# Optimization experiments

Measured on AMD Instinct MI355X. Metric: run time of the kernel, lower is better.

Reference implementation:

```python
import jax, jax.numpy as jnp
import numpy as np

B, N, F_DIM = 64, 4096, 64
K_SLOTS, D, N_ITERS = 8, 64, 3
EPS = 1e-8
LN_EPS = 1e-5  # torch LayerNorm default


def layernorm(x, g, b):
    mu = jnp.mean(x, axis=-1, keepdims=True)
    var = jnp.mean(jnp.square(x - mu), axis=-1, keepdims=True)
    return (x - mu) * jax.lax.rsqrt(var + LN_EPS) * g + b


def gru_cell(x, h, w_ih, w_hh, b_ih, b_hh):
    # torch.nn.GRUCell semantics; weights are [3D, D] with gate order r, z, n
    gi = x @ w_ih.T + b_ih
    gh = h @ w_hh.T + b_hh
    i_r, i_z, i_n = jnp.split(gi, 3, axis=-1)
    h_r, h_z, h_n = jnp.split(gh, 3, axis=-1)
    r = jax.nn.sigmoid(i_r + h_r)
    z = jax.nn.sigmoid(i_z + h_z)
    n = jnp.tanh(i_n + r * h_n)
    return (1.0 - z) * n + z * h


def setup_inputs() -> dict:
    key = jax.random.key(0)
    ks = jax.random.split(key, 16)
    f32 = jnp.float32
    s = 0.05  # small init scale for weights
    return {
        "inputs": jax.random.normal(ks[0], (B, N, F_DIM), f32),
        "slots_noise": jax.random.normal(ks[1], (B, K_SLOTS, D), f32),
        "slots_mu": jax.random.normal(ks[2], (1, 1, D), f32) * s,
        "slots_log_sigma": jax.random.normal(ks[3], (1, 1, D), f32) * s,
        "Wq": jax.random.normal(ks[4], (D, D), f32) * s,
        "Wk": jax.random.normal(ks[5], (D, F_DIM), f32) * s,
        "Wv": jax.random.normal(ks[6], (D, F_DIM), f32) * s,
        "gru_w_ih": jax.random.normal(ks[7], (3 * D, D), f32) * s,
        "gru_w_hh": jax.random.normal(ks[8], (3 * D, D), f32) * s,
        "gru_b_ih": jnp.zeros((3 * D,), f32),
        "gru_b_hh": jnp.zeros((3 * D,), f32),
        "mlp_w1": jax.random.normal(ks[9], (2 * D, D), f32) * s,
        "mlp_b1": jnp.zeros((2 * D,), f32),
        "mlp_w2": jax.random.normal(ks[10], (D, 2 * D), f32) * s,
        "mlp_b2": jnp.zeros((D,), f32),
        "ln_in_g": jnp.ones((F_DIM,), f32), "ln_in_b": jnp.zeros((F_DIM,), f32),
        "ln_slots_g": jnp.ones((D,), f32), "ln_slots_b": jnp.zeros((D,), f32),
        "ln_mlp_g": jnp.ones((D,), f32), "ln_mlp_b": jnp.zeros((D,), f32),
    }


def reference(inputs, slots_noise, slots_mu, slots_log_sigma, Wq, Wk, Wv,
              gru_w_ih, gru_w_hh, gru_b_ih, gru_b_hh,
              mlp_w1, mlp_b1, mlp_w2, mlp_b2,
              ln_in_g, ln_in_b, ln_slots_g, ln_slots_b, ln_mlp_g, ln_mlp_b):
    x = layernorm(inputs, ln_in_g, ln_in_b)          # [B, N, F]
    k = jnp.einsum('bnf,df->bnd', x, Wk)             # [B, N, D]
    v = jnp.einsum('bnf,df->bnd', x, Wv)             # [B, N, D]

    slots = slots_mu + jnp.exp(slots_log_sigma) * slots_noise  # [B, K, D]
    scale = D ** -0.5

    for _ in range(N_ITERS):
        slots_prev = slots
        s_n = layernorm(slots, ln_slots_g, ln_slots_b)
        q = jnp.einsum('bkd,ed->bke', s_n, Wq)                  # [B, K, D]
        attn_logits = jnp.einsum('bnd,bkd->bnk', k, q) * scale  # [B, N, K]
        attn = jax.nn.softmax(attn_logits, axis=-1) + EPS       # softmax over slots
        attn = attn / jnp.sum(attn, axis=1, keepdims=True)      # renormalize over N
        updates = jnp.einsum('bnk,bnd->bkd', attn, v)           # [B, K, D]
        slots = gru_cell(updates.reshape(-1, D), slots_prev.reshape(-1, D),
                         gru_w_ih, gru_w_hh, gru_b_ih, gru_b_hh).reshape(B, K_SLOTS, D)
        h = layernorm(slots, ln_mlp_g, ln_mlp_b)
        h = jax.nn.relu(h @ mlp_w1.T + mlp_b1) @ mlp_w2.T + mlp_b2
        slots = slots + h
    return slots
```

## Files before the change

### kernel.cpp

```cpp
#include <hip/hip_runtime.h>
#include <math.h>

#define NN 4096
#define LN_EPS 1e-5f
#define EPS 1e-8f

typedef unsigned short ushortT;
typedef unsigned int uintT;
typedef __attribute__((ext_vector_type(8))) short short8;
typedef __attribute__((ext_vector_type(4))) float f32x4;
typedef __attribute__((ext_vector_type(4))) unsigned short us4;

#define OFF_KT    0L
#define OFF_V     16777216L
#define OFF_QT    33554432L
#define OFF_PART  33587200L
#define OFF_PCOL  34111488L
#define OFF_SLOTS 34119680L
#define OFF_WIHT  34152448L
#define OFF_WHHT  34164736L
#define OFF_W1T   34177024L
#define OFF_W2T   34185216L
#define OFF_WQT   34193408L
#define OFF_WKV   34197504L
#define OFF_CNT   34201600L

__device__ __forceinline__ float wredsum(float v) {
#pragma unroll
  for (int off = 32; off > 0; off >>= 1) v += __shfl_xor(v, off);
  return v;
}

__device__ __forceinline__ ushortT f2bf(float f) {
  uintT b = __float_as_uint(f);
  b += 0x7fff + ((b >> 16) & 1);
  return (ushortT)(b >> 16);
}

__global__ __launch_bounds__(256) void k_setup(
    const float* __restrict__ w_ih, const float* __restrict__ w_hh,
    const float* __restrict__ w1, const float* __restrict__ w2,
    const float* __restrict__ Wq,
    const float* __restrict__ Wk, const float* __restrict__ Wv,
    const float* __restrict__ noise, const float* __restrict__ smu,
    const float* __restrict__ slsig,
    const float* __restrict__ g_sl, const float* __restrict__ b_sl,
    float* __restrict__ wihT, float* __restrict__ whhT,
    float* __restrict__ w1T, float* __restrict__ w2T, float* __restrict__ wqT,
    ushortT* __restrict__ wpack,
    float* __restrict__ slots, ushortT* __restrict__ qF,
    int* __restrict__ cnt)
{
  const int tid = threadIdx.x;
  int idx = blockIdx.x * 256 + tid;
  if (idx < 12288) {
    int j = idx >> 6, f = idx & 63;
    wihT[f * 192 + j] = w_ih[idx];
  } else if (idx < 24576) {
    int i = idx - 12288; int j = i >> 6, f = i & 63;
    whhT[f * 192 + j] = w_hh[i];
  } else if (idx < 32768) {
    int i = idx - 24576; int j = i >> 6, f = i & 63;
    w1T[f * 128 + j] = w1[i];
  } else if (idx < 40960) {
    int i = idx - 32768; int d = i >> 7, j = i & 127;
    w2T[j * 64 + d] = w2[i];
  } else if (idx < 45056) {
    int i = idx - 40960; int e = i >> 6, d = i & 63;
    wqT[d * 64 + e] = Wq[i];
  } else if (idx < 53248) {
    int i = idx - 45056;
    int j = i & 7, l = (i >> 3) & 63, t2 = i >> 9;
    int ct = t2 >> 1, kb = t2 & 1;
    int kf = kb * 32 + ((l >> 4) << 3) + j;
    int col = (ct << 4) | (l & 15);
    float val = (col < 64) ? Wk[col * 64 + kf] : Wv[(col - 64) * 64 + kf];
    wpack[i] = f2bf(val);
  }

  if (blockIdx.x >= 128) {
    if (blockIdx.x < 136) cnt[(blockIdx.x - 128) * 256 + tid] = 0;
    return;
  }

  __shared__ float WqS[64 * 65];
  __shared__ float S[4][64];
  const int lane = tid & 63, wave = tid >> 6;
  const int row = blockIdx.x * 4 + wave;
  const int b = row >> 3, ks = row & 7;

#pragma unroll
  for (int i = 0; i < 16; ++i) {
    int ii = tid + i * 256;
    int e = ii >> 6, d = ii & 63;
    WqS[d * 65 + e] = Wq[ii];
  }

  float s0 = fmaf(expf(slsig[lane]), noise[row * 64 + lane], smu[lane]);
  slots[row * 64 + lane] = s0;

  float mu = wredsum(s0) * (1.f / 64.f);
  float dx = s0 - mu;
  float var = wredsum(dx * dx) * (1.f / 64.f);
  float sn = dx * rsqrtf(var + LN_EPS) * g_sl[lane] + b_sl[lane];
  S[wave][lane] = sn;
  __syncthreads();
  float qe = 0.f;
#pragma unroll 16
  for (int d = 0; d < 64; ++d) qe = fmaf(S[wave][d], WqS[d * 65 + lane], qe);
  const int kb = lane >> 5, lrow = (lane & 31) >> 3, j = lane & 7;
  qF[((((b * 2 + kb) << 6) + (lrow << 4) + ks) << 3) + j] = f2bf(qe * 0.125f);
  qF[((((b * 2 + kb) << 6) + (lrow << 4) + 8 + ks) << 3) + j] = 0;
}

__global__ __launch_bounds__(256, 4) void k_ln_project(
    const float* __restrict__ inp, const ushortT* __restrict__ wpack,
    const float* __restrict__ g, const float* __restrict__ bbv,
    ushortT* __restrict__ ktF, ushortT* __restrict__ vF)
{
  __shared__ __align__(16) ushortT xnF[4096];
  __shared__ __align__(16) ushortT kS[4096];
  const int tid = threadIdx.x;
  const int lane = tid & 63;
  const int wave = tid >> 6;
  const int l15 = lane & 15, q = lane >> 4;
  const int tile = blockIdx.x;
  const int b = tile >> 6;
  const int c = tile & 63;
  const int n0 = c << 6;
  const float* rowbase = inp + (((long)b * NN + n0) << 6);
  const float4 g4 = *(const float4*)&g[l15 << 2];
  const float4 b4 = *(const float4*)&bbv[l15 << 2];

#pragma unroll
  for (int i = 0; i < 4; ++i) {
    const int row = (wave << 4) + (i << 2) + q;
    float4 x = *(const float4*)&rowbase[(row << 6) + (l15 << 2)];
    float s = x.x + x.y + x.z + x.w;
    float s2 = fmaf(x.x, x.x, fmaf(x.y, x.y, fmaf(x.z, x.z, x.w * x.w)));
    s += __shfl_xor(s, 1);  s2 += __shfl_xor(s2, 1);
    s += __shfl_xor(s, 2);  s2 += __shfl_xor(s2, 2);
    s += __shfl_xor(s, 4);  s2 += __shfl_xor(s2, 4);
    s += __shfl_xor(s, 8);  s2 += __shfl_xor(s2, 8);
    const float mu = s * (1.f / 64.f);
    const float var = fmaf(-mu, mu, s2 * (1.f / 64.f));
    const float rs = rsqrtf(var + LN_EPS);
    us4 p = {f2bf((x.x - mu) * rs * g4.x + b4.x), f2bf((x.y - mu) * rs * g4.y + b4.y),
             f2bf((x.z - mu) * rs * g4.z + b4.z), f2bf((x.w - mu) * rs * g4.w + b4.w)};
    *(us4*)&xnF[((((wave << 1) + (l15 >> 3)) << 6) + (((l15 & 7) >> 1) << 4)
                 + (row & 15)) * 8 + ((l15 & 1) << 2)] = p;
  }

  short8 bfrag[2][2];
#pragma unroll
  for (int nt = 0; nt < 2; ++nt)
#pragma unroll
    for (int kb = 0; kb < 2; ++kb)
      bfrag[nt][kb] = *(const short8*)&wpack[((((2 * wave + nt) << 1) | kb) * 64 + lane) << 3];

  __syncthreads();

  f32x4 acc[4][2];
#pragma unroll
  for (int mt = 0; mt < 4; ++mt)
#pragma unroll
    for (int nt = 0; nt < 2; ++nt) acc[mt][nt] = (f32x4){0.f, 0.f, 0.f, 0.f};

#pragma unroll
  for (int mt = 0; mt < 4; ++mt) {
    short8 a0 = *(const short8*)&xnF[((mt * 2 + 0) * 64 + lane) << 3];
    short8 a1 = *(const short8*)&xnF[((mt * 2 + 1) * 64 + lane) << 3];
#pragma unroll
    for (int nt = 0; nt < 2; ++nt) {
      acc[mt][nt] = __builtin_amdgcn_mfma_f32_16x16x32_bf16(a0, bfrag[nt][0], acc[mt][nt], 0, 0, 0);
      acc[mt][nt] = __builtin_amdgcn_mfma_f32_16x16x32_bf16(a1, bfrag[nt][1], acc[mt][nt], 0, 0, 0);
    }
  }

  if (wave < 2) {
#pragma unroll
    for (int mt = 0; mt < 4; ++mt)
#pragma unroll
      for (int nt = 0; nt < 2; ++nt) {
        const int base = (((mt * 2 + wave) << 6) + ((2 * nt + (l15 >> 3)) << 4) + (q << 2));
#pragma unroll
        for (int r = 0; r < 4; ++r)
          kS[((base + r) << 3) + (l15 & 7)] = f2bf(acc[mt][nt][r]);
      }
  } else {
    ushortT* vbase = vF + ((long)(b * 64 + c) << 12);
#pragma unroll
    for (int mt = 0; mt < 4; ++mt)
#pragma unroll
      for (int nt = 0; nt < 2; ++nt) {
        const int ntg = 2 * (wave - 2) + nt;
        us4 p = {f2bf(acc[mt][nt][0]), f2bf(acc[mt][nt][1]),
                 f2bf(acc[mt][nt][2]), f2bf(acc[mt][nt][3])};
        *(us4*)&vbase[(((((ntg << 1) + (mt >> 1)) << 6)
                        + (((mt & 1) * 2 + (q >> 1)) << 4) + l15) << 3)
                      + ((q & 1) << 2)] = p;
      }
  }
  __syncthreads();

  ushortT* kdst = ktF + ((long)(b * 64 + c) << 12);
  short8 v0 = *(const short8*)&kS[tid << 4];
  short8 v1 = *(const short8*)&kS[(tid << 4) + 8];
  *(short8*)&kdst[tid << 4] = v0;
  *(short8*)&kdst[(tid << 4) + 8] = v1;
}

__global__ __launch_bounds__(256, 4) void k_attn_fused(
    const ushortT* __restrict__ ktF, const ushortT* __restrict__ vF,
    ushortT* __restrict__ qF,
    float* __restrict__ part, float* __restrict__ pcol, int* __restrict__ cnt,
    float* __restrict__ slots,
    const float* __restrict__ wihT, const float* __restrict__ whhT,
    const float* __restrict__ w1T, const float* __restrict__ w2T,
    const float* __restrict__ wqT,
    const float* __restrict__ b_ih, const float* __restrict__ b_hh,
    const float* __restrict__ mb1, const float* __restrict__ mb2,
    const float* __restrict__ g_ml, const float* __restrict__ b_ml,
    const float* __restrict__ g_sl, const float* __restrict__ b_sl,
    float* __restrict__ dout, int it)
{
  __shared__ __align__(16) ushortT attnF[4][1024];
  __shared__ float redLds[4][512];
  __shared__ float colLds[4][8];
  __shared__ int flagS;
  const int tid = threadIdx.x;
  const int lane = tid & 63;
  const int wave = tid >> 6;
  const int l15 = lane & 15, q = lane >> 4;
  const int b = blockIdx.x >> 4;
  const int i16 = blockIdx.x & 15;
  const int chunk = (i16 << 2) | wave;

  const ushortT* kbF = ktF + ((long)(b * 64 + chunk) << 12);
  const ushortT* vbF = vF + ((long)(b * 64 + chunk) << 12);

  short8 qB[2];
#pragma unroll
  for (int kb = 0; kb < 2; ++kb)
    qB[kb] = *(const short8*)&qF[(((b * 2 + kb) << 6) + lane) << 3];
  short8 kA[4][2];
#pragma unroll
  for (int mt = 0; mt < 4; ++mt)
#pragma unroll
    for (int kb = 0; kb < 2; ++kb)
      kA[mt][kb] = *(const short8*)&kbF[((mt * 2 + kb) * 64 + lane) << 3];
  short8 vB[4][2];
#pragma unroll
  for (int nt = 0; nt < 4; ++nt)
#pragma unroll
    for (int ks = 0; ks < 2; ++ks)
      vB[nt][ks] = *(const short8*)&vbF[((nt * 2 + ks) * 64 + lane) << 3];

  f32x4 accL[4];
#pragma unroll
  for (int mt = 0; mt < 4; ++mt) {
    accL[mt] = (f32x4){0.f, 0.f, 0.f, 0.f};
    accL[mt] = __builtin_amdgcn_mfma_f32_16x16x32_bf16(kA[mt][0], qB[0], accL[mt], 0, 0, 0);
    accL[mt] = __builtin_amdgcn_mfma_f32_16x16x32_bf16(kA[mt][1], qB[1], accL[mt], 0, 0, 0);
  }

  float csum = 0.f;
#pragma unroll
  for (int mt = 0; mt < 4; ++mt) {
    float av[4];
#pragma unroll
    for (int r = 0; r < 4; ++r) {
      float ev = __expf(accL[mt][r]);
      float sv = ev;
      sv += __shfl_xor(sv, 1); sv += __shfl_xor(sv, 2); sv += __shfl_xor(sv, 4);
      float a = ev * (1.f / sv) + EPS;
      av[r] = a;
      csum += a;
    }
    us4 p = {f2bf(av[0]), f2bf(av[1]), f2bf(av[2]), f2bf(av[3])};
    *(us4*)&attnF[wave][((((mt >> 1) << 6) + (((mt & 1) * 2 + (q >> 1)) << 4)
                          + l15) << 3) + ((q & 1) << 2)] = p;
  }
  csum += __shfl_xor(csum, 16);
  csum += __shfl_xor(csum, 32);

  short8 pA0 = *(const short8*)&attnF[wave][(0 * 64 + lane) << 3];
  short8 pA1 = *(const short8*)&attnF[wave][(1 * 64 + lane) << 3];

  f32x4 accP[4];
#pragma unroll
  for (int nt = 0; nt < 4; ++nt) {
    accP[nt] = (f32x4){0.f, 0.f, 0.f, 0.f};
    accP[nt] = __builtin_amdgcn_mfma_f32_16x16x32_bf16(pA0, vB[nt][0], accP[nt], 0, 0, 0);
    accP[nt] = __builtin_amdgcn_mfma_f32_16x16x32_bf16(pA1, vB[nt][1], accP[nt], 0, 0, 0);
  }

  float (*accLds)[8][64] = (float (*)[8][64])redLds;
  if (q < 2) {
#pragma unroll
    for (int nt = 0; nt < 4; ++nt)
#pragma unroll
      for (int r = 0; r < 4; ++r)
        accLds[wave][q * 4 + r][nt * 16 + l15] = accP[nt][r];
  }
  if (q == 0 && l15 < 8) colLds[wave][l15] = csum;
  __syncthreads();

  float* myPart = part + ((long)(b * 16 + i16) << 9);
#pragma unroll
  for (int r = 0; r < 2; ++r) {
    const int o = tid + r * 256;
    const int kk = o >> 6, d = o & 63;
    float s = accLds[0][kk][d] + accLds[1][kk][d] + accLds[2][kk][d] + accLds[3][kk][d];
    __hip_atomic_store(&myPart[o], s, __ATOMIC_RELAXED, __HIP_MEMORY_SCOPE_AGENT);
  }
  if (tid < 8) {
    float s = colLds[0][tid] + colLds[1][tid] + colLds[2][tid] + colLds[3][tid];
    __hip_atomic_store(&pcol[(b * 16 + i16) * 8 + tid], s,
                       __ATOMIC_RELAXED, __HIP_MEMORY_SCOPE_AGENT);
  }

  asm volatile("s_waitcnt vmcnt(0) lgkmcnt(0)" ::: "memory");
  __syncthreads();
  if (tid == 0) {
    int old = atomicAdd(&cnt[b << 5], 1);
    flagS = (old == it * 16 + 15);
  }
  __syncthreads();
  if (!flagS) return;

  float* accR = (float*)&attnF[0][0];
  float* csR  = accR + 512;
  const float* partB = part + ((long)b << 13);
#pragma unroll
  for (int r = 0; r < 2; ++r) {
    const int o = tid + r * 256;
    float s = 0.f;
#pragma unroll
    for (int i = 0; i < 16; ++i)
      s += __hip_atomic_load(&partB[(i << 9) + o], __ATOMIC_RELAXED, __HIP_MEMORY_SCOPE_AGENT);
    accR[o] = s;
  }
  if (tid < 8) {
    float s = 0.f;
#pragma unroll
    for (int i = 0; i < 16; ++i)
      s += __hip_atomic_load(&pcol[(b * 16 + i) * 8 + tid], __ATOMIC_RELAXED, __HIP_MEMORY_SCOPE_AGENT);
    csR[tid] = s;
  }
  __syncthreads();

  float* SwA = &redLds[wave][0];
  float* SwB = &redLds[wave][256];
  const int ksA = wave * 2, ksB = ksA + 1;
  const int rowA = b * 8 + ksA, rowB = b * 8 + ksB;

  const float bir = b_ih[lane], biz = b_ih[64 + lane], bin_ = b_ih[128 + lane];
  const float bhr = b_hh[lane], bhz = b_hh[64 + lane], bhn = b_hh[128 + lane];
  const float m1a = mb1[lane], m1b = mb1[64 + lane];
  const float m2v = mb2[lane];
  const float gml = g_ml[lane], bml = b_ml[lane];
  const float gsl = g_sl[lane], bsl = b_sl[lane];

  const float u0 = accR[ksA * 64 + lane] / csR[ksA];
  const float u1 = accR[ksB * 64 + lane] / csR[ksB];
  const float h0 = slots[rowA * 64 + lane];
  const float h1 = slots[rowB * 64 + lane];
  SwA[lane] = u0; SwA[64 + lane] = h0;
  SwB[lane] = u1; SwB[64 + lane] = h1;

  float gir0 = bir, giz0 = biz, gin0 = bin_, ghr0 = bhr, ghz0 = bhz, ghn0 = bhn;
  float gir1 = bir, giz1 = biz, gin1 = bin_, ghr1 = bhr, ghz1 = bhz, ghn1 = bhn;
#pragma unroll 8
  for (int f = 0; f < 64; ++f) {
    const float wr = wihT[f * 192 + lane], wz = wihT[f * 192 + 64 + lane],
                wn = wihT[f * 192 + 128 + lane];
    const float vr = whhT[f * 192 + lane], vz = whhT[f * 192 + 64 + lane],
                vn = whhT[f * 192 + 128 + lane];
    const float uA = SwA[f], hA = SwA[64 + f];
    const float uB = SwB[f], hB = SwB[64 + f];
    gir0 = fmaf(uA, wr, gir0); giz0 = fmaf(uA, wz, giz0); gin0 = fmaf(uA, wn, gin0);
    ghr0 = fmaf(hA, vr, ghr0); ghz0 = fmaf(hA, vz, ghz0); ghn0 = fmaf(hA, vn, ghn0);
    gir1 = fmaf(uB, wr, gir1); giz1 = fmaf(uB, wz, giz1); gin1 = fmaf(uB, wn, gin1);
    ghr1 = fmaf(hB, vr, ghr1); ghz1 = fmaf(hB, vz, ghz1); ghn1 = fmaf(hB, vn, ghn1);
  }
  const float r0 = 1.f / (1.f + expf(-(gir0 + ghr0)));
  const float z0 = 1.f / (1.f + expf(-(giz0 + ghz0)));
  const float n0v = tanhf(fmaf(r0, ghn0, gin0));
  const float hnew0 = (1.f - z0) * n0v + z0 * h0;
  const float r1 = 1.f / (1.f + expf(-(gir1 + ghr1)));
  const float z1 = 1.f / (1.f + expf(-(giz1 + ghz1)));
  const float n1v = tanhf(fmaf(r1, ghn1, gin1));
  const float hnew1 = (1.f - z1) * n1v + z1 * h1;

  float sa = hnew0, sb = hnew1;
#pragma unroll
  for (int off = 32; off > 0; off >>= 1) { sa += __shfl_xor(sa, off); sb += __shfl_xor(sb, off); }
  const float muA = sa * (1.f / 64.f), muB = sb * (1.f / 64.f);
  float dxA = hnew0 - muA, dxB = hnew1 - muB;
  float va = dxA * dxA, vb = dxB * dxB;
#pragma unroll
  for (int off = 32; off > 0; off >>= 1) { va += __shfl_xor(va, off); vb += __shfl_xor(vb, off); }
  SwA[128 + lane] = dxA * rsqrtf(va * (1.f / 64.f) + LN_EPS) * gml + bml;
  SwB[128 + lane] = dxB * rsqrtf(vb * (1.f / 64.f) + LN_EPS) * gml + bml;

  float h1a0 = m1a, h1b0 = m1b, h1a1 = m1a, h1b1 = m1b;
#pragma unroll 8
  for (int f = 0; f < 64; ++f) {
    const float wA = w1T[f * 128 + lane], wB = w1T[f * 128 + 64 + lane];
    const float lA = SwA[128 + f], lB = SwB[128 + f];
    h1a0 = fmaf(lA, wA, h1a0); h1b0 = fmaf(lA, wB, h1b0);
    h1a1 = fmaf(lB, wA, h1a1); h1b1 = fmaf(lB, wB, h1b1);
  }
  SwA[lane] = fmaxf(h1a0, 0.f); SwA[64 + lane] = fmaxf(h1b0, 0.f);
  SwB[lane] = fmaxf(h1a1, 0.f); SwB[64 + lane] = fmaxf(h1b1, 0.f);

  float o0 = m2v, o1 = m2v;
#pragma unroll 8
  for (int j = 0; j < 128; ++j) {
    const float w = w2T[j * 64 + lane];
    o0 = fmaf(SwA[j], w, o0);
    o1 = fmaf(SwB[j], w, o1);
  }
  const float snew0 = hnew0 + o0;
  const float snew1 = hnew1 + o1;
  slots[rowA * 64 + lane] = snew0;
  slots[rowB * 64 + lane] = snew1;
  if (dout) { dout[rowA * 64 + lane] = snew0; dout[rowB * 64 + lane] = snew1; }

  float ta = snew0, tb = snew1;
#pragma unroll
  for (int off = 32; off > 0; off >>= 1) { ta += __shfl_xor(ta, off); tb += __shfl_xor(tb, off); }
  const float mu2A = ta * (1.f / 64.f), mu2B = tb * (1.f / 64.f);
  float d2A = snew0 - mu2A, d2B = snew1 - mu2B;
  float v2a = d2A * d2A, v2b = d2B * d2B;
#pragma unroll
  for (int off = 32; off > 0; off >>= 1) { v2a += __shfl_xor(v2a, off); v2b += __shfl_xor(v2b, off); }
  SwA[128 + lane] = d2A * rsqrtf(v2a * (1.f / 64.f) + LN_EPS) * gsl + bsl;
  SwB[128 + lane] = d2B * rsqrtf(v2b * (1.f / 64.f) + LN_EPS) * gsl + bsl;

  float qe0 = 0.f, qe1 = 0.f;
#pragma unroll 8
  for (int d = 0; d < 64; ++d) {
    const float w = wqT[d * 64 + lane];
    qe0 = fmaf(SwA[128 + d], w, qe0);
    qe1 = fmaf(SwB[128 + d], w, qe1);
  }
  const int kb = lane >> 5, lrow = (lane & 31) >> 3, j = lane & 7;
  qF[((((b * 2 + kb) << 6) + (lrow << 4) + ksA) << 3) + j] = f2bf(qe0 * 0.125f);
  qF[((((b * 2 + kb) << 6) + (lrow << 4) + ksB) << 3) + j] = f2bf(qe1 * 0.125f);
}

extern "C" void kernel_launch(void* const* d_in, const int* in_sizes, int n_in,
                              void* d_out, int out_size, void* d_ws, size_t ws_size,
                              hipStream_t stream) {
  const float* inp   = (const float*)d_in[0];
  const float* noise = (const float*)d_in[1];
  const float* smu   = (const float*)d_in[2];
  const float* slsig = (const float*)d_in[3];
  const float* Wq    = (const float*)d_in[4];
  const float* Wk    = (const float*)d_in[5];
  const float* Wv    = (const float*)d_in[6];
  const float* w_ih  = (const float*)d_in[7];
  const float* w_hh  = (const float*)d_in[8];
  const float* b_ih  = (const float*)d_in[9];
  const float* b_hh  = (const float*)d_in[10];
  const float* w1    = (const float*)d_in[11];
  const float* b1    = (const float*)d_in[12];
  const float* w2    = (const float*)d_in[13];
  const float* b2    = (const float*)d_in[14];
  const float* g_in  = (const float*)d_in[15];
  const float* bi_in = (const float*)d_in[16];
  const float* g_sl  = (const float*)d_in[17];
  const float* bi_sl = (const float*)d_in[18];
  const float* g_ml  = (const float*)d_in[19];
  const float* bi_ml = (const float*)d_in[20];

  float* ws      = (float*)d_ws;
  ushortT* ktF   = (ushortT*)(ws + OFF_KT);
  ushortT* vF    = (ushortT*)(ws + OFF_V);
  ushortT* qF    = (ushortT*)(ws + OFF_QT);
  float* part    = ws + OFF_PART;
  float* pcol    = ws + OFF_PCOL;
  float* sl      = ws + OFF_SLOTS;
  float* wihT    = ws + OFF_WIHT;
  float* whhT    = ws + OFF_WHHT;
  float* w1T     = ws + OFF_W1T;
  float* w2T     = ws + OFF_W2T;
  float* wqT     = ws + OFF_WQT;
  ushortT* wpk   = (ushortT*)(ws + OFF_WKV);
  int* cnt       = (int*)(ws + OFF_CNT);

  k_setup<<<208, 256, 0, stream>>>(w_ih, w_hh, w1, w2, Wq, Wk, Wv,
                                   noise, smu, slsig, g_sl, bi_sl,
                                   wihT, whhT, w1T, w2T, wqT, wpk,
                                   sl, qF, cnt);
  k_ln_project<<<4096, 256, 0, stream>>>(inp, wpk, g_in, bi_in, ktF, vF);
  for (int it = 0; it < 3; ++it) {
    k_attn_fused<<<1024, 256, 0, stream>>>(ktF, vF, qF, part, pcol, cnt, sl,
                                           wihT, whhT, w1T, w2T, wqT,
                                           b_ih, b_hh, b1, b2, g_ml, bi_ml, g_sl, bi_sl,
                                           it == 2 ? (float*)d_out : nullptr, it);
  }
}
```

Baseline: 250.5 us.

## Fuse three slot-attention iterations into one persistent kernel with per-batch flags

Result: slower. 438.9 us (+75.2%).

```diff
diff --git a/kernel.cpp b/kernel.cpp
--- a/kernel.cpp
+++ b/kernel.cpp
@@ -79,7 +79,7 @@
   }
 
   if (blockIdx.x >= 128) {
-    if (blockIdx.x < 136) cnt[(blockIdx.x - 128) * 256 + tid] = 0;
+    if (blockIdx.x < 144) cnt[(blockIdx.x - 128) * 256 + tid] = 0;
     return;
   }
 
@@ -210,9 +210,9 @@
   *(short8*)&kdst[(tid << 4) + 8] = v1;
 }
 
-__global__ __launch_bounds__(256, 4) void k_attn_fused(
+__global__ __launch_bounds__(256, 4) void k_attn_iter(
     const ushortT* __restrict__ ktF, const ushortT* __restrict__ vF,
-    ushortT* __restrict__ qF,
+    const ushortT* __restrict__ qF,
     float* __restrict__ part, float* __restrict__ pcol, int* __restrict__ cnt,
     float* __restrict__ slots,
     const float* __restrict__ wihT, const float* __restrict__ whhT,
@@ -222,7 +222,7 @@
     const float* __restrict__ mb1, const float* __restrict__ mb2,
     const float* __restrict__ g_ml, const float* __restrict__ b_ml,
     const float* __restrict__ g_sl, const float* __restrict__ b_sl,
-    float* __restrict__ dout, int it)
+    float* __restrict__ dout)
 {
   __shared__ __align__(16) ushortT attnF[4][1024];
   __shared__ float redLds[4][512];
@@ -238,11 +238,10 @@
 
   const ushortT* kbF = ktF + ((long)(b * 64 + chunk) << 12);
   const ushortT* vbF = vF + ((long)(b * 64 + chunk) << 12);
-
-  short8 qB[2];
-#pragma unroll
-  for (int kb = 0; kb < 2; ++kb)
-    qB[kb] = *(const short8*)&qF[(((b * 2 + kb) << 6) + lane) << 3];
+  int* cnt_b = &cnt[b << 5];
+  int* flg_b = &cnt[2048 + (b << 5)];
+  const float gsl = g_sl[lane], bsl = b_sl[lane];
+
   short8 kA[4][2];
 #pragma unroll
   for (int mt = 0; mt < 4; ++mt)
@@ -256,199 +255,245 @@
     for (int ks = 0; ks < 2; ++ks)
       vB[nt][ks] = *(const short8*)&vbF[((nt * 2 + ks) * 64 + lane) << 3];
 
-  f32x4 accL[4];
-#pragma unroll
-  for (int mt = 0; mt < 4; ++mt) {
-    accL[mt] = (f32x4){0.f, 0.f, 0.f, 0.f};
-    accL[mt] = __builtin_amdgcn_mfma_f32_16x16x32_bf16(kA[mt][0], qB[0], accL[mt], 0, 0, 0);
-    accL[mt] = __builtin_amdgcn_mfma_f32_16x16x32_bf16(kA[mt][1], qB[1], accL[mt], 0, 0, 0);
-  }
-
-  float csum = 0.f;
-#pragma unroll
-  for (int mt = 0; mt < 4; ++mt) {
-    float av[4];
-#pragma unroll
-    for (int r = 0; r < 4; ++r) {
-      float ev = __expf(accL[mt][r]);
-      float sv = ev;
-      sv += __shfl_xor(sv, 1); sv += __shfl_xor(sv, 2); sv += __shfl_xor(sv, 4);
-      float a = ev * (1.f / sv) + EPS;
-      av[r] = a;
-      csum += a;
-    }
-    us4 p = {f2bf(av[0]), f2bf(av[1]), f2bf(av[2]), f2bf(av[3])};
-    *(us4*)&attnF[wave][((((mt >> 1) << 6) + (((mt & 1) * 2 + (q >> 1)) << 4)
-                          + l15) << 3) + ((q & 1) << 2)] = p;
-  }
-  csum += __shfl_xor(csum, 16);
-  csum += __shfl_xor(csum, 32);
-
-  short8 pA0 = *(const short8*)&attnF[wave][(0 * 64 + lane) << 3];
-  short8 pA1 = *(const short8*)&attnF[wave][(1 * 64 + lane) << 3];
-
-  f32x4 accP[4];
-#pragma unroll
-  for (int nt = 0; nt < 4; ++nt) {
-    accP[nt] = (f32x4){0.f, 0.f, 0.f, 0.f};
-    accP[nt] = __builtin_amdgcn_mfma_f32_16x16x32_bf16(pA0, vB[nt][0], accP[nt], 0, 0, 0);
-    accP[nt] = __builtin_amdgcn_mfma_f32_16x16x32_bf16(pA1, vB[nt][1], accP[nt], 0, 0, 0);
-  }
-
-  float (*accLds)[8][64] = (float (*)[8][64])redLds;
-  if (q < 2) {
-#pragma unroll
-    for (int nt = 0; nt < 4; ++nt)
-#pragma unroll
-      for (int r = 0; r < 4; ++r)
-        accLds[wave][q * 4 + r][nt * 16 + l15] = accP[nt][r];
-  }
-  if (q == 0 && l15 < 8) colLds[wave][l15] = csum;
-  __syncthreads();
-
-  float* myPart = part + ((long)(b * 16 + i16) << 9);
-#pragma unroll
-  for (int r = 0; r < 2; ++r) {
-    const int o = tid + r * 256;
-    const int kk = o >> 6, d = o & 63;
-    float s = accLds[0][kk][d] + accLds[1][kk][d] + accLds[2][kk][d] + accLds[3][kk][d];
-    __hip_atomic_store(&myPart[o], s, __ATOMIC_RELAXED, __HIP_MEMORY_SCOPE_AGENT);
-  }
-  if (tid < 8) {
-    float s = colLds[0][tid] + colLds[1][tid] + colLds[2][tid] + colLds[3][tid];
-    __hip_atomic_store(&pcol[(b * 16 + i16) * 8 + tid], s,
-                       __ATOMIC_RELAXED, __HIP_MEMORY_SCOPE_AGENT);
-  }
-
-  asm volatile("s_waitcnt vmcnt(0) lgkmcnt(0)" ::: "memory");
-  __syncthreads();
-  if (tid == 0) {
-    int old = atomicAdd(&cnt[b << 5], 1);
-    flagS = (old == it * 16 + 15);
-  }
-  __syncthreads();
-  if (!flagS) return;
-
-  float* accR = (float*)&attnF[0][0];
-  float* csR  = accR + 512;
-  const float* partB = part + ((long)b << 13);
-#pragma unroll
-  for (int r = 0; r < 2; ++r) {
-    const int o = tid + r * 256;
-    float s = 0.f;
-#pragma unroll
-    for (int i = 0; i < 16; ++i)
-      s += __hip_atomic_load(&partB[(i << 9) + o], __ATOMIC_RELAXED, __HIP_MEMORY_SCOPE_AGENT);
-    accR[o] = s;
-  }
-  if (tid < 8) {
-    float s = 0.f;
-#pragma unroll
-    for (int i = 0; i < 16; ++i)
-      s += __hip_atomic_load(&pcol[(b * 16 + i) * 8 + tid], __ATOMIC_RELAXED, __HIP_MEMORY_SCOPE_AGENT);
-    csR[tid] = s;
-  }
-  __syncthreads();
-
-  float* SwA = &redLds[wave][0];
-  float* SwB = &redLds[wave][256];
-  const int ksA = wave * 2, ksB = ksA + 1;
-  const int rowA = b * 8 + ksA, rowB = b * 8 + ksB;
-
-  const float bir = b_ih[lane], biz = b_ih[64 + lane], bin_ = b_ih[128 + lane];
-  const float bhr = b_hh[lane], bhz = b_hh[64 + lane], bhn = b_hh[128 + lane];
-  const float m1a = mb1[lane], m1b = mb1[64 + lane];
-  const float m2v = mb2[lane];
-  const float gml = g_ml[lane], bml = b_ml[lane];
-  const float gsl = g_sl[lane], bsl = b_sl[lane];
-
-  const float u0 = accR[ksA * 64 + lane] / csR[ksA];
-  const float u1 = accR[ksB * 64 + lane] / csR[ksB];
-  const float h0 = slots[rowA * 64 + lane];
-  const float h1 = slots[rowB * 64 + lane];
-  SwA[lane] = u0; SwA[64 + lane] = h0;
-  SwB[lane] = u1; SwB[64 + lane] = h1;
-
-  float gir0 = bir, giz0 = biz, gin0 = bin_, ghr0 = bhr, ghz0 = bhz, ghn0 = bhn;
-  float gir1 = bir, giz1 = biz, gin1 = bin_, ghr1 = bhr, ghz1 = bhz, ghn1 = bhn;
+  for (int it = 0; it < 3; ++it) {
+    short8 qB[2];
+    if (it == 0) {
+#pragma unroll
+      for (int kb = 0; kb < 2; ++kb)
+        qB[kb] = *(const short8*)&qF[(((b * 2 + kb) << 6) + lane) << 3];
+    } else {
+      if (tid == 0) {
+        while (__hip_atomic_load(flg_b, __ATOMIC_RELAXED, __HIP_MEMORY_SCOPE_AGENT) < it)
+          __builtin_amdgcn_s_sleep(2);
+      }
+      __syncthreads();
+      float* qsq  = &redLds[0][0];
+      float* qLds = &redLds[2][0];
+      const int ksA = wave * 2, ksB = ksA + 1;
+      float sA = __hip_atomic_load(&slots[(b * 8 + ksA) * 64 + lane],
+                                   __ATOMIC_RELAXED, __HIP_MEMORY_SCOPE_AGENT);
+      float sB = __hip_atomic_load(&slots[(b * 8 + ksB) * 64 + lane],
+                                   __ATOMIC_RELAXED, __HIP_MEMORY_SCOPE_AGENT);
+      float ta = sA, tb = sB;
+#pragma unroll
+      for (int off = 32; off > 0; off >>= 1) { ta += __shfl_xor(ta, off); tb += __shfl_xor(tb, off); }
+      const float muA = ta * (1.f / 64.f), muB = tb * (1.f / 64.f);
+      const float dxA = sA - muA, dxB = sB - muB;
+      float va = dxA * dxA, vb = dxB * dxB;
+#pragma unroll
+      for (int off = 32; off > 0; off >>= 1) { va += __shfl_xor(va, off); vb += __shfl_xor(vb, off); }
+      qsq[ksA * 64 + lane] = dxA * rsqrtf(va * (1.f / 64.f) + LN_EPS) * gsl + bsl;
+      qsq[ksB * 64 + lane] = dxB * rsqrtf(vb * (1.f / 64.f) + LN_EPS) * gsl + bsl;
+      __syncthreads();
+      float qeA = 0.f, qeB = 0.f;
 #pragma unroll 8
-  for (int f = 0; f < 64; ++f) {
-    const float wr = wihT[f * 192 + lane], wz = wihT[f * 192 + 64 + lane],
-                wn = wihT[f * 192 + 128 + lane];
-    const float vr = whhT[f * 192 + lane], vz = whhT[f * 192 + 64 + lane],
-                vn = whhT[f * 192 + 128 + lane];
-    const float uA = SwA[f], hA = SwA[64 + f];
-    const float uB = SwB[f], hB = SwB[64 + f];
-    gir0 = fmaf(uA, wr, gir0); giz0 = fmaf(uA, wz, giz0); gin0 = fmaf(uA, wn, gin0);
-    ghr0 = fmaf(hA, vr, ghr0); ghz0 = fmaf(hA, vz, ghz0); ghn0 = fmaf(hA, vn, ghn0);
-    gir1 = fmaf(uB, wr, gir1); giz1 = fmaf(uB, wz, giz1); gin1 = fmaf(uB, wn, gin1);
-    ghr1 = fmaf(hB, vr, ghr1); ghz1 = fmaf(hB, vz, ghz1); ghn1 = fmaf(hB, vn, ghn1);
-  }
-  const float r0 = 1.f / (1.f + expf(-(gir0 + ghr0)));
-  const float z0 = 1.f / (1.f + expf(-(giz0 + ghz0)));
-  const float n0v = tanhf(fmaf(r0, ghn0, gin0));
-  const float hnew0 = (1.f - z0) * n0v + z0 * h0;
-  const float r1 = 1.f / (1.f + expf(-(gir1 + ghr1)));
-  const float z1 = 1.f / (1.f + expf(-(giz1 + ghz1)));
-  const float n1v = tanhf(fmaf(r1, ghn1, gin1));
-  const float hnew1 = (1.f - z1) * n1v + z1 * h1;
-
-  float sa = hnew0, sb = hnew1;
-#pragma unroll
-  for (int off = 32; off > 0; off >>= 1) { sa += __shfl_xor(sa, off); sb += __shfl_xor(sb, off); }
-  const float muA = sa * (1.f / 64.f), muB = sb * (1.f / 64.f);
-  float dxA = hnew0 - muA, dxB = hnew1 - muB;
-  float va = dxA * dxA, vb = dxB * dxB;
-#pragma unroll
-  for (int off = 32; off > 0; off >>= 1) { va += __shfl_xor(va, off); vb += __shfl_xor(vb, off); }
-  SwA[128 + lane] = dxA * rsqrtf(va * (1.f / 64.f) + LN_EPS) * gml + bml;
-  SwB[128 + lane] = dxB * rsqrtf(vb * (1.f / 64.f) + LN_EPS) * gml + bml;
-
-  float h1a0 = m1a, h1b0 = m1b, h1a1 = m1a, h1b1 = m1b;
+      for (int d = 0; d < 64; ++d) {
+        const float w = wqT[d * 64 + lane];
+        qeA = fmaf(qsq[ksA * 64 + d], w, qeA);
+        qeB = fmaf(qsq[ksB * 64 + d], w, qeB);
+      }
+      qLds[ksA * 64 + lane] = qeA * 0.125f;
+      qLds[ksB * 64 + lane] = qeB * 0.125f;
+      __syncthreads();
+#pragma unroll
+      for (int kb = 0; kb < 2; ++kb) {
+        short8 v = (short8){0, 0, 0, 0, 0, 0, 0, 0};
+        if (l15 < 8) {
+          const int e0 = (kb << 5) + (q << 3);
+          float4 f0 = *(const float4*)&qLds[l15 * 64 + e0];
+          float4 f1 = *(const float4*)&qLds[l15 * 64 + e0 + 4];
+          v[0] = (short)f2bf(f0.x); v[1] = (short)f2bf(f0.y);
+          v[2] = (short)f2bf(f0.z); v[3] = (short)f2bf(f0.w);
+          v[4] = (short)f2bf(f1.x); v[5] = (short)f2bf(f1.y);
+          v[6] = (short)f2bf(f1.z); v[7] = (short)f2bf(f1.w);
+        }
+        qB[kb] = v;
+      }
+      __syncthreads();
+    }
+
+    f32x4 accL[4];
+#pragma unroll
+    for (int mt = 0; mt < 4; ++mt) {
+      accL[mt] = (f32x4){0.f, 0.f, 0.f, 0.f};
+      accL[mt] = __builtin_amdgcn_mfma_f32_16x16x32_bf16(kA[mt][0], qB[0], accL[mt], 0, 0, 0);
+      accL[mt] = __builtin_amdgcn_mfma_f32_16x16x32_bf16(kA[mt][1], qB[1], accL[mt], 0, 0, 0);
+    }
+
+    float csum = 0.f;
+#pragma unroll
+    for (int mt = 0; mt < 4; ++mt) {
+      float av[4];
+#pragma unroll
+      for (int r = 0; r < 4; ++r) {
+        float ev = __expf(accL[mt][r]);
+        float sv = ev;
+        sv += __shfl_xor(sv, 1); sv += __shfl_xor(sv, 2); sv += __shfl_xor(sv, 4);
+        float a = ev * (1.f / sv) + EPS;
+        av[r] = a;
+        csum += a;
+      }
+      us4 p = {f2bf(av[0]), f2bf(av[1]), f2bf(av[2]), f2bf(av[3])};
+      *(us4*)&attnF[wave][((((mt >> 1) << 6) + (((mt & 1) * 2 + (q >> 1)) << 4)
+                            + l15) << 3) + ((q & 1) << 2)] = p;
+    }
+    csum += __shfl_xor(csum, 16);
+    csum += __shfl_xor(csum, 32);
+
+    short8 pA0 = *(const short8*)&attnF[wave][(0 * 64 + lane) << 3];
+    short8 pA1 = *(const short8*)&attnF[wave][(1 * 64 + lane) << 3];
+
+    f32x4 accP[4];
+#pragma unroll
+    for (int nt = 0; nt < 4; ++nt) {
+      accP[nt] = (f32x4){0.f, 0.f, 0.f, 0.f};
+      accP[nt] = __builtin_amdgcn_mfma_f32_16x16x32_bf16(pA0, vB[nt][0], accP[nt], 0, 0, 0);
+      accP[nt] = __builtin_amdgcn_mfma_f32_16x16x32_bf16(pA1, vB[nt][1], accP[nt], 0, 0, 0);
+    }
+
+    float (*accLds)[8][64] = (float (*)[8][64])redLds;
+    if (q < 2) {
+#pragma unroll
+      for (int nt = 0; nt < 4; ++nt)
+#pragma unroll
+        for (int r = 0; r < 4; ++r)
+          accLds[wave][q * 4 + r][nt * 16 + l15] = accP[nt][r];
+    }
+    if (q == 0 && l15 < 8) colLds[wave][l15] = csum;
+    __syncthreads();
+
+    float* myPart = part + ((long)(b * 16 + i16) << 9);
+#pragma unroll
+    for (int r = 0; r < 2; ++r) {
+      const int o = tid + r * 256;
+      const int kk = o >> 6, d = o & 63;
+      float s = accLds[0][kk][d] + accLds[1][kk][d] + accLds[2][kk][d] + accLds[3][kk][d];
+      __hip_atomic_store(&myPart[o], s, __ATOMIC_RELAXED, __HIP_MEMORY_SCOPE_AGENT);
+    }
+    if (tid < 8) {
+      float s = colLds[0][tid] + colLds[1][tid] + colLds[2][tid] + colLds[3][tid];
+      __hip_atomic_store(&pcol[(b * 16 + i16) * 8 + tid], s,
+                         __ATOMIC_RELAXED, __HIP_MEMORY_SCOPE_AGENT);
+    }
+
+    asm volatile("s_waitcnt vmcnt(0) lgkmcnt(0)" ::: "memory");
+    __syncthreads();
+    if (tid == 0) {
+      int old = atomicAdd(cnt_b, 1);
+      flagS = (old == it * 16 + 15);
+    }
+    __syncthreads();
+
+    if (flagS) {
+      float* accR = (float*)&attnF[0][0];
+      float* csR  = accR + 512;
+      const float* partB = part + ((long)b << 13);
+#pragma unroll
+      for (int r = 0; r < 2; ++r) {
+        const int o = tid + r * 256;
+        float s = 0.f;
+#pragma unroll
+        for (int i = 0; i < 16; ++i)
+          s += __hip_atomic_load(&partB[(i << 9) + o], __ATOMIC_RELAXED, __HIP_MEMORY_SCOPE_AGENT);
+        accR[o] = s;
+      }
+      if (tid < 8) {
+        float s = 0.f;
+#pragma unroll
+        for (int i = 0; i < 16; ++i)
+          s += __hip_atomic_load(&pcol[(b * 16 + i) * 8 + tid], __ATOMIC_RELAXED, __HIP_MEMORY_SCOPE_AGENT);
+        csR[tid] = s;
+      }
+      __syncthreads();
+
+      float* SwA = &redLds[wave][0];
+      float* SwB = &redLds[wave][256];
+      const int ksA = wave * 2, ksB = ksA + 1;
+      const int rowA = b * 8 + ksA, rowB = b * 8 + ksB;
+
+      const float bir = b_ih[lane], biz = b_ih[64 + lane], bin_ = b_ih[128 + lane];
+      const float bhr = b_hh[lane], bhz = b_hh[64 + lane], bhn = b_hh[128 + lane];
+      const float m1a = mb1[lane], m1b = mb1[64 + lane];
+      const float m2v = mb2[lane];
+      const float gml = g_ml[lane], bml = b_ml[lane];
+
+      const float u0 = accR[ksA * 64 + lane] / csR[ksA];
+      const float u1 = accR[ksB * 64 + lane] / csR[ksB];
+      const float h0 = __hip_atomic_load(&slots[rowA * 64 + lane], __ATOMIC_RELAXED, __HIP_MEMORY_SCOPE_AGENT);
+      const float h1 = __hip_atomic_load(&slots[rowB * 64 + lane], __ATOMIC_RELAXED, __HIP_MEMORY_SCOPE_AGENT);
+      SwA[lane] = u0; SwA[64 + lane] = h0;
+      SwB[lane] = u1; SwB[64 + lane] = h1;
+
+      float gir0 = bir, giz0 = biz, gin0 = bin_, ghr0 = bhr, ghz0 = bhz, ghn0 = bhn;
+      float gir1 = bir, giz1 = biz, gin1 = bin_, ghr1 = bhr, ghz1 = bhz, ghn1 = bhn;
 #pragma unroll 8
-  for (int f = 0; f < 64; ++f) {
-    const float wA = w1T[f * 128 + lane], wB = w1T[f * 128 + 64 + lane];
-    const float lA = SwA[128 + f], lB = SwB[128 + f];
-    h1a0 = fmaf(lA, wA, h1a0); h1b0 = fmaf(lA, wB, h1b0);
-    h1a1 = fmaf(lB, wA, h1a1); h1b1 = fmaf(lB, wB, h1b1);
-  }
-  SwA[lane] = fmaxf(h1a0, 0.f); SwA[64 + lane] = fmaxf(h1b0, 0.f);
-  SwB[lane] = fmaxf(h1a1, 0.f); SwB[64 + lane] = fmaxf(h1b1, 0.f);
-
-  float o0 = m2v, o1 = m2v;
+      for (int f = 0; f < 64; ++f) {
+        const float wr = wihT[f * 192 + lane], wz = wihT[f * 192 + 64 + lane],
+                    wn = wihT[f * 192 + 128 + lane];
+        const float vr = whhT[f * 192 + lane], vz = whhT[f * 192 + 64 + lane],
+                    vn = whhT[f * 192 + 128 + lane];
+        const float uA = SwA[f], hA = SwA[64 + f];
+        const float uB = SwB[f], hB = SwB[64 + f];
+        gir0 = fmaf(uA, wr, gir0); giz0 = fmaf(uA, wz, giz0); gin0 = fmaf(uA, wn, gin0);
+        ghr0 = fmaf(hA, vr, ghr0); ghz0 = fmaf(hA, vz, ghz0); ghn0 = fmaf(hA, vn, ghn0);
+        gir1 = fmaf(uB, wr, gir1); giz1 = fmaf(uB, wz, giz1); gin1 = fmaf(uB, wn, gin1);
+        ghr1 = fmaf(hB, vr, ghr1); ghz1 = fmaf(hB, vz, ghz1); ghn1 = fmaf(hB, vn, ghn1);
+      }
+      const float r0 = 1.f / (1.f + expf(-(gir0 + ghr0)));
+      const float z0 = 1.f / (1.f + expf(-(giz0 + ghz0)));
+      const float n0v = tanhf(fmaf(r0, ghn0, gin0));
+      const float hnew0 = (1.f - z0) * n0v + z0 * h0;
+      const float r1 = 1.f / (1.f + expf(-(gir1 + ghr1)));
+      const float z1 = 1.f / (1.f + expf(-(giz1 + ghz1)));
+      const float n1v = tanhf(fmaf(r1, ghn1, gin1));
+      const float hnew1 = (1.f - z1) * n1v + z1 * h1;
+
+      float sa = hnew0, sb = hnew1;
+#pragma unroll
+      for (int off = 32; off > 0; off >>= 1) { sa += __shfl_xor(sa, off); sb += __shfl_xor(sb, off); }
+      const float muA = sa * (1.f / 64.f), muB = sb * (1.f / 64.f);
+      float dxA = hnew0 - muA, dxB = hnew1 - muB;
+      float va = dxA * dxA, vb = dxB * dxB;
+#pragma unroll
+      for (int off = 32; off > 0; off >>= 1) { va += __shfl_xor(va, off); vb += __shfl_xor(vb, off); }
+      SwA[128 + lane] = dxA * rsqrtf(va * (1.f / 64.f) + LN_EPS) * gml + bml;
+      SwB[128 + lane] = dxB * rsqrtf(vb * (1.f / 64.f) + LN_EPS) * gml + bml;
+
+      float h1a0 = m1a, h1b0 = m1b, h1a1 = m1a, h1b1 = m1b;
 #pragma unroll 8
-  for (int j = 0; j < 128; ++j) {
-    const float w = w2T[j * 64 + lane];
-    o0 = fmaf(SwA[j], w, o0);
-    o1 = fmaf(SwB[j], w, o1);
-  }
-  const float snew0 = hnew0 + o0;
-  const float snew1 = hnew1 + o1;
-  slots[rowA * 64 + lane] = snew0;
-  slots[rowB * 64 + lane] = snew1;
-  if (dout) { dout[rowA * 64 + lane] = snew0; dout[rowB * 64 + lane] = snew1; }
-
-  float ta = snew0, tb = snew1;
-#pragma unroll
-  for (int off = 32; off > 0; off >>= 1) { ta += __shfl_xor(ta, off); tb += __shfl_xor(tb, off); }
-  const float mu2A = ta * (1.f / 64.f), mu2B = tb * (1.f / 64.f);
-  float d2A = snew0 - mu2A, d2B = snew1 - mu2B;
-  float v2a = d2A * d2A, v2b = d2B * d2B;
-#pragma unroll
-  for (int off = 32; off > 0; off >>= 1) { v2a += __shfl_xor(v2a, off); v2b += __shfl_xor(v2b, off); }
-  SwA[128 + lane] = d2A * rsqrtf(v2a * (1.f / 64.f) + LN_EPS) * gsl + bsl;
-  SwB[128 + lane] = d2B * rsqrtf(v2b * (1.f / 64.f) + LN_EPS) * gsl + bsl;
-
-  float qe0 = 0.f, qe1 = 0.f;
+      for (int f = 0; f < 64; ++f) {
+        const float wA = w1T[f * 128 + lane], wB = w1T[f * 128 + 64 + lane];
+        const float lA = SwA[128 + f], lB = SwB[128 + f];
+        h1a0 = fmaf(lA, wA, h1a0); h1b0 = fmaf(lA, wB, h1b0);
+        h1a1 = fmaf(lB, wA, h1a1); h1b1 = fmaf(lB, wB, h1b1);
+      }
+      SwA[lane] = fmaxf(h1a0, 0.f); SwA[64 + lane] = fmaxf(h1b0, 0.f);
+      SwB[lane] = fmaxf(h1a1, 0.f); SwB[64 + lane] = fmaxf(h1b1, 0.f);
+
+      float o0 = m2v, o1 = m2v;
 #pragma unroll 8
-  for (int d = 0; d < 64; ++d) {
-    const float w = wqT[d * 64 + lane];
-    qe0 = fmaf(SwA[128 + d], w, qe0);
-    qe1 = fmaf(SwB[128 + d], w, qe1);
-  }
-  const int kb = lane >> 5, lrow = (lane & 31) >> 3, j = lane & 7;
-  qF[((((b * 2 + kb) << 6) + (lrow << 4) + ksA) << 3) + j] = f2bf(qe0 * 0.125f);
-  qF[((((b * 2 + kb) << 6) + (lrow << 4) + ksB) << 3) + j] = f2bf(qe1 * 0.125f);
+      for (int j = 0; j < 128; ++j) {
+        const float w = w2T[j * 64 + lane];
+        o0 = fmaf(SwA[j], w, o0);
+        o1 = fmaf(SwB[j], w, o1);
+      }
+      const float snew0 = hnew0 + o0;
+      const float snew1 = hnew1 + o1;
+
+      if (it == 2) {
+        dout[rowA * 64 + lane] = snew0;
+        dout[rowB * 64 + lane] = snew1;
+      } else {
+        __hip_atomic_store(&slots[rowA * 64 + lane], snew0, __ATOMIC_RELAXED, __HIP_MEMORY_SCOPE_AGENT);
+        __hip_atomic_store(&slots[rowB * 64 + lane], snew1, __ATOMIC_RELAXED, __HIP_MEMORY_SCOPE_AGENT);
+        asm volatile("s_waitcnt vmcnt(0) lgkmcnt(0)" ::: "memory");
+        __syncthreads();
+        if (tid == 0)
+          __hip_atomic_store(flg_b, it + 1, __ATOMIC_RELAXED, __HIP_MEMORY_SCOPE_AGENT);
+      }
+    }
+    if (it == 2) break;
+  }
 }
 
 extern "C" void kernel_launch(void* const* d_in, const int* in_sizes, int n_in,
@@ -496,10 +541,8 @@
                                    wihT, whhT, w1T, w2T, wqT, wpk,
                                    sl, qF, cnt);
   k_ln_project<<<4096, 256, 0, stream>>>(inp, wpk, g_in, bi_in, ktF, vF);
-  for (int it = 0; it < 3; ++it) {
-    k_attn_fused<<<1024, 256, 0, stream>>>(ktF, vF, qF, part, pcol, cnt, sl,
-                                           wihT, whhT, w1T, w2T, wqT,
-                                           b_ih, b_hh, b1, b2, g_ml, bi_ml, g_sl, bi_sl,
-                                           it == 2 ? (float*)d_out : nullptr, it);
-  }
+  k_attn_iter<<<1024, 256, 0, stream>>>(ktF, vF, qF, part, pcol, cnt, sl,
+                                        wihT, whhT, w1T, w2T, wqT,
+                                        b_ih, b_hh, b1, b2, g_ml, bi_ml, g_sl, bi_sl,
+                                        (float*)d_out);
 }
```
